# Performance work log

Measured on AMD Instinct MI355X. Metric: run time of the kernel, lower is better.

The kernel has to match this reference:

```python
import jax, jax.numpy as jnp
import numpy as np

H = 4          # num_heads (= num_kv_heads, num_kv_groups = 1)
DK = 256       # head_k_dim
DV = 256       # head_v_dim
M = 256        # num_slots
GATE_NORM = 16.0
EPS = 1e-5


def _rmsnorm(x, w):
    var = jnp.mean(jnp.square(x), axis=-1, keepdims=True)
    return x * jax.lax.rsqrt(var + EPS) * w


def _swish(x):
    return x * jax.nn.sigmoid(x)


def setup_inputs() -> dict:
    key = jax.random.key(0)
    ks = jax.random.split(key, 8)
    B, T, D = 4, 2048, 1024
    scale = 2 ** (-2.5) * (2.0 / (D + D)) ** 0.5 * (3.0 ** 0.5) * 2  # ~xavier*gain magnitude
    return {
        "hidden_states": jax.random.normal(ks[0], (B, T, D), jnp.float32),
        "norm_weight": jnp.ones((D,), jnp.float32),
        "w_q": jax.random.normal(ks[1], (D, D), jnp.float32) * scale,
        "w_k": jax.random.normal(ks[2], (D, D), jnp.float32) * scale,
        "w_v": jax.random.normal(ks[3], (D, D), jnp.float32) * scale,
        "w_f": jax.random.normal(ks[4], (H * M, D), jnp.float32) * scale,
        "gnorm_weight": jnp.ones((D,), jnp.float32),
        "w_o": jax.random.normal(ks[5], (D, D), jnp.float32) * scale,
    }


def _gsa_scan(q, k, v, s, g):
    # all inputs time-major: q [T,B,H,DK], k [T,B,H,DK], v [T,B,H,DV],
    # s [T,B,H,M] (slot write strength), g [T,B,H,M] (log forget gate)
    B, Hh = q.shape[1], q.shape[2]
    Hk0 = jnp.zeros((B, Hh, DK, M), q.dtype)
    Hv0 = jnp.zeros((B, Hh, M, DV), q.dtype)

    def step(carry, xs):
        Hk, Hv = carry
        qt, kt, vt, st, gt = xs
        lam = jnp.exp(gt)                                       # [B,H,M]
        # pass 1: linear attn over slots (gate on value/slot dim)
        Hk = Hk * lam[:, :, None, :] + kt[..., :, None] * st[..., None, :]
        z = jnp.einsum('bhk,bhkm->bhm', qt, Hk)                 # slot logits
        p = jax.nn.softmax(z, axis=-1)                          # slot read weights
        # pass 2: linear attn from slots to values (gate on key/slot dim)
        Hv = Hv * lam[..., :, None] + st[..., :, None] * vt[..., None, :]
        ot = jnp.einsum('bhm,bhmv->bhv', p, Hv)
        return (Hk, Hv), ot

    _, o = jax.lax.scan(step, (Hk0, Hv0), (q, k, v, s, g))
    return o  # [T,B,H,DV]


def reference(hidden_states, norm_weight, w_q, w_k, w_v, w_f, gnorm_weight, w_o):
    B, T, D = hidden_states.shape
    h = _rmsnorm(hidden_states, norm_weight)                    # norm_first
    q = _swish(h @ w_q.T).reshape(B, T, H, DK)                  # swish feature map
    k = _swish(h @ w_k.T).reshape(B, T, H, DK)
    v = _swish(h @ w_v.T).reshape(B, T, H, DV)
    f = jax.nn.log_sigmoid(h @ w_f.T).reshape(B, T, H, M) / GATE_NORM
    s = 1.0 - jnp.exp(f)
    tm = lambda x: jnp.transpose(x, (1, 0, 2, 3))               # [B,T,H,*] -> [T,B,H,*]
    o = _gsa_scan(tm(q), tm(k), tm(v), tm(s), tm(f))            # [T,B,H,DV]
    o = jnp.transpose(o, (1, 0, 2, 3)).reshape(B, T, H * DV)
    # use_norm & no output gate: swish -> RMSNorm -> o_proj
    o = _swish(o)
    o = _rmsnorm(o, gnorm_weight)
    return o @ w_o.T
```

## Files before the change

### kernel.cpp

```cpp
#include <hip/hip_runtime.h>
#include <hip/hip_bf16.h>

typedef unsigned short u16;
typedef unsigned int u32;

using bf16x8 = __bf16 __attribute__((ext_vector_type(8)));
using s16x8  = short  __attribute__((ext_vector_type(8)));
using f32x4  = float  __attribute__((ext_vector_type(4)));

#define DEV static __device__ __forceinline__

constexpr int T_ = 2048, D_ = 1024;
constexpr int C_ = 64, NC_ = 32;
constexpr float EPS_ = 1e-5f;

DEV float bf2f(u16 u) { return __uint_as_float(((u32)u) << 16); }
DEV u16 f2bf(float f) {
  u32 u = __float_as_uint(f);
  return (u16)((u + 0x7fffu + ((u >> 16) & 1u)) >> 16);
}
DEV float swishf(float x) { return x / (1.f + __expf(-x)); }
DEV f32x4 zero4() { f32x4 z = {0.f, 0.f, 0.f, 0.f}; return z; }

DEV bf16x8 ld8(const u16* p, int ld, int r0, int k0, int lane) {
  return *(const bf16x8*)(p + (size_t)(r0 + (lane & 15)) * ld +
                          (size_t)(k0 + ((lane >> 4) << 3)));
}
DEV f32x4 MFMA(bf16x8 a, bf16x8 b, f32x4 c) {
  return __builtin_amdgcn_mfma_f32_16x16x32_bf16(a, b, c, 0, 0, 0);
}
DEV void gld_lds16(const void* g, void* l) {
  __builtin_amdgcn_global_load_lds(
      (const __attribute__((address_space(1))) unsigned int*)g,
      (__attribute__((address_space(3))) unsigned int*)l, 16, 0, 0);
}

__global__ __launch_bounds__(256) void k_cvt5(
    const float* __restrict__ s0, const float* __restrict__ s1,
    const float* __restrict__ s2, const float* __restrict__ s3,
    const float* __restrict__ s4, u16* __restrict__ d0, u16* __restrict__ d1,
    u16* __restrict__ d2, u16* __restrict__ d3, u16* __restrict__ d4) {
  const int wsel = blockIdx.x >> 10;
  const float* s = (wsel == 0) ? s0 : (wsel == 1) ? s1 : (wsel == 2) ? s2
                   : (wsel == 3) ? s3 : s4;
  u16* d = (wsel == 0) ? d0 : (wsel == 1) ? d1 : (wsel == 2) ? d2
           : (wsel == 3) ? d3 : d4;
  const int i = (blockIdx.x & 1023) * 256 + threadIdx.x;
  float4 v = ((const float4*)s)[i];
  uint2 o;
  o.x = (u32)f2bf(v.x) | ((u32)f2bf(v.y) << 16);
  o.y = (u32)f2bf(v.z) | ((u32)f2bf(v.w) << 16);
  ((uint2*)d)[i] = o;
}

__global__ __launch_bounds__(256) void k_rmsnorm(const float* __restrict__ x,
                                                 const float* __restrict__ w,
                                                 u16* __restrict__ h) {
  const int row = blockIdx.x, tid = threadIdx.x;
  float4 v = ((const float4*)(x + (size_t)row * D_))[tid];
  float ss = v.x * v.x + v.y * v.y + v.z * v.z + v.w * v.w;
#pragma unroll
  for (int d = 32; d >= 1; d >>= 1) ss += __shfl_xor(ss, d, 64);
  __shared__ float red[4];
  if ((tid & 63) == 0) red[tid >> 6] = ss;
  __syncthreads();
  float rs = rsqrtf((red[0] + red[1] + red[2] + red[3]) * (1.f / D_) + EPS_);
  float4 wv = ((const float4*)w)[tid];
  uint2 o;
  o.x = (u32)f2bf(v.x * rs * wv.x) | ((u32)f2bf(v.y * rs * wv.y) << 16);
  o.y = (u32)f2bf(v.z * rs * wv.z) | ((u32)f2bf(v.w * rs * wv.w) << 16);
  *(uint2*)(h + (size_t)row * D_ + tid * 4) = o;
}

__global__ __launch_bounds__(256) void k_swishnorm(const u16* __restrict__ x,
                                                   const float* __restrict__ w,
                                                   u16* __restrict__ o) {
  const int row = blockIdx.x, tid = threadIdx.x;
  uint2 pk = *(const uint2*)(x + (size_t)row * D_ + tid * 4);
  float v0 = swishf(bf2f((u16)(pk.x & 0xffff))), v1 = swishf(bf2f((u16)(pk.x >> 16)));
  float v2 = swishf(bf2f((u16)(pk.y & 0xffff))), v3 = swishf(bf2f((u16)(pk.y >> 16)));
  float ss = v0 * v0 + v1 * v1 + v2 * v2 + v3 * v3;
#pragma unroll
  for (int d = 32; d >= 1; d >>= 1) ss += __shfl_xor(ss, d, 64);
  __shared__ float red[4];
  if ((tid & 63) == 0) red[tid >> 6] = ss;
  __syncthreads();
  float rs = rsqrtf((red[0] + red[1] + red[2] + red[3]) * (1.f / D_) + EPS_);
  float4 wv = ((const float4*)w)[tid];
  uint2 ov;
  ov.x = (u32)f2bf(v0 * rs * wv.x) | ((u32)f2bf(v1 * rs * wv.y) << 16);
  ov.y = (u32)f2bf(v2 * rs * wv.z) | ((u32)f2bf(v3 * rs * wv.w) << 16);
  *(uint2*)(o + (size_t)row * D_ + tid * 4) = ov;
}

__global__ __launch_bounds__(256, 2) void k_gemm4(
    const u16* __restrict__ A, const u16* __restrict__ w0,
    const u16* __restrict__ w1, const u16* __restrict__ w2,
    const u16* __restrict__ w3, u16* __restrict__ oq, u16* __restrict__ okk,
    u16* __restrict__ ov, float* __restrict__ og) {
  __shared__ __align__(16) u16 As[128 * 32];
  __shared__ __align__(16) u16 Bs[4][64 * 32];
  const int m0 = blockIdx.x * 128, n0 = blockIdx.y * 64;
  const int tid = threadIdx.x, lane = tid & 63, wvi = tid >> 6;
  f32x4 acc[4][2][4];
#pragma unroll
  for (int w = 0; w < 4; w++)
#pragma unroll
    for (int i = 0; i < 2; i++)
#pragma unroll
      for (int j = 0; j < 4; j++) acc[w][i][j] = zero4();
  const int srow = tid >> 2, scb = (tid & 3) * 8;
  const u16* Ag = A + (size_t)(m0 + srow) * 1024 + scb;
  const u16* Wg0 = w0 + (size_t)(n0 + srow) * 1024 + scb;
  const u16* Wg1 = w1 + (size_t)(n0 + srow) * 1024 + scb;
  const u16* Wg2 = w2 + (size_t)(n0 + srow) * 1024 + scb;
  const u16* Wg3 = w3 + (size_t)(n0 + srow) * 1024 + scb;
  u16* AsW = As + (wvi * 16) * 32;
  const int bofs = (wvi * 16) * 32;
  for (int kk = 0; kk < 1024; kk += 32) {
    gld_lds16(Ag + kk, AsW);
    gld_lds16(Ag + kk + 64 * 1024, AsW + 64 * 32);
    gld_lds16(Wg0 + kk, Bs[0] + bofs);
    gld_lds16(Wg1 + kk, Bs[1] + bofs);
    gld_lds16(Wg2 + kk, Bs[2] + bofs);
    gld_lds16(Wg3 + kk, Bs[3] + bofs);
    __syncthreads();
    bf16x8 af[2];
#pragma unroll
    for (int i = 0; i < 2; i++) af[i] = ld8(As, 32, wvi * 32 + 16 * i, 0, lane);
#pragma unroll
    for (int w = 0; w < 4; w++) {
      bf16x8 bfr[4];
#pragma unroll
      for (int j = 0; j < 4; j++) bfr[j] = ld8(Bs[w], 32, 16 * j, 0, lane);
#pragma unroll
      for (int i = 0; i < 2; i++)
#pragma unroll
        for (int j = 0; j < 4; j++) acc[w][i][j] = MFMA(af[i], bfr[j], acc[w][i][j]);
    }
    __syncthreads();
  }
  const int q4 = lane >> 4, c15 = lane & 15;
#pragma unroll
  for (int w = 0; w < 4; w++)
#pragma unroll
    for (int i = 0; i < 2; i++)
#pragma unroll
      for (int j = 0; j < 4; j++)
#pragma unroll
        for (int r = 0; r < 4; r++) {
          int grow = m0 + wvi * 32 + 16 * i + 4 * q4 + r;
          int gcol = n0 + 16 * j + c15;
          size_t idx = (size_t)grow * 1024 + gcol;
          float val = acc[w][i][j][r];
          if (w < 3) {
            u16* o = (w == 0) ? oq : (w == 1) ? okk : ov;
            o[idx] = f2bf(swishf(val));
          } else {
            float g = (val >= 0.f) ? -log1pf(__expf(-val))
                                   : (val - log1pf(__expf(val)));
            og[idx] = g * (1.0f / 16.0f);
          }
        }
}

__global__ __launch_bounds__(256) void k_gemmO(const u16* __restrict__ A,
                                               const u16* __restrict__ W,
                                               float* __restrict__ ofin) {
  __shared__ __align__(16) u16 As[128 * 32];
  __shared__ __align__(16) u16 Bs[128 * 32];
  const int m0 = blockIdx.x * 128, n0 = blockIdx.y * 128;
  const int tid = threadIdx.x, lane = tid & 63, wvi = tid >> 6;
  const int wr = wvi >> 1, wc = wvi & 1;
  f32x4 acc[4][4];
#pragma unroll
  for (int i = 0; i < 4; i++)
#pragma unroll
    for (int j = 0; j < 4; j++) acc[i][j] = zero4();
  const int srow = tid >> 2, scb = (tid & 3) * 8;
  const u16* Ag = A + (size_t)(m0 + srow) * 1024 + scb;
  const u16* Wg = W + (size_t)(n0 + srow) * 1024 + scb;
  u16* AsW = As + (wvi * 16) * 32;
  u16* BsW = Bs + (wvi * 16) * 32;
  for (int kk = 0; kk < 1024; kk += 32) {
    gld_lds16(Ag + kk, AsW);
    gld_lds16(Ag + kk + 64 * 1024, AsW + 64 * 32);
    gld_lds16(Wg + kk, BsW);
    gld_lds16(Wg + kk + 64 * 1024, BsW + 64 * 32);
    __syncthreads();
    bf16x8 af[4], bfr[4];
#pragma unroll
    for (int i = 0; i < 4; i++) af[i] = ld8(As, 32, wr * 64 + 16 * i, 0, lane);
#pragma unroll
    for (int j = 0; j < 4; j++) bfr[j] = ld8(Bs, 32, wc * 64 + 16 * j, 0, lane);
#pragma unroll
    for (int i = 0; i < 4; i++)
#pragma unroll
      for (int j = 0; j < 4; j++) acc[i][j] = MFMA(af[i], bfr[j], acc[i][j]);
    __syncthreads();
  }
  const int q4 = lane >> 4, c15 = lane & 15;
#pragma unroll
  for (int i = 0; i < 4; i++)
#pragma unroll
    for (int j = 0; j < 4; j++)
#pragma unroll
      for (int r = 0; r < 4; r++) {
        int grow = m0 + wr * 64 + 16 * i + 4 * q4 + r;
        int gcol = n0 + wc * 64 + 16 * j + c15;
        ofin[(size_t)grow * 1024 + gcol] = acc[i][j][r];
      }
}

__global__ __launch_bounds__(256) void k_gates(float* __restrict__ g_inout,
                                               u16* __restrict__ U_t,
                                               float* __restrict__ Lam) {
  const int c = blockIdx.x, p = blockIdx.y, tid = threadIdx.x;
  const int b = p >> 2, hh = p & 3;
  const int R0 = b * T_ + c * C_, hb = hh * 256;
  float ga = 0.f, ea = 1.f;
  short ubuf[C_];
#pragma unroll
  for (int t = 0; t < C_; t++) {
    size_t gi = (size_t)(R0 + t) * D_ + hb + tid;
    float gv = g_inout[gi];
    ga += gv;
    ea = __expf(ga);
    ubuf[t] = (short)f2bf((1.f - __expf(gv)) * __expf(-ga));
    g_inout[gi] = ea;
  }
  Lam[((size_t)p * NC_ + c) * 256 + tid] = ea;
  u16* up = U_t + ((size_t)p * NC_ + c) * (256 * C_) + (size_t)tid * C_;
#pragma unroll
  for (int i = 0; i < 8; i++) {
    s16x8 w;
#pragma unroll
    for (int j = 0; j < 8; j++) w[j] = ubuf[i * 8 + j];
    *(s16x8*)(up + i * 8) = w;
  }
}

__global__ __launch_bounds__(256) void k_intra(
    const u16* __restrict__ kg, const u16* __restrict__ vg,
    const u16* __restrict__ U_t, const float* __restrict__ Lam,
    u16* __restrict__ Sk, u16* __restrict__ Sv) {
  __shared__ __align__(16) u16 KV[256 * 72];
  __shared__ float LamH[256];
  const int c = blockIdx.x, p = blockIdx.y;
  const int b = p >> 2, hh = p & 3;
  const int R0 = b * T_ + c * C_, hb = hh * 256;
  const int tid = threadIdx.x, lane = tid & 63, wvi = tid >> 6;
  const int q4 = lane >> 4, c15 = lane & 15;
  const size_t chunk = (size_t)p * NC_ + c;
  const u16* Uc = U_t + chunk * (256 * C_);
  const size_t scBase = chunk * (256 * 256);

  LamH[tid] = Lam[chunk * 256 + tid];
  for (int t = 0; t < C_; t++)
    KV[tid * 72 + t] = kg[(size_t)(R0 + t) * D_ + hb + tid];
  __syncthreads();

  for (int cb = 0; cb < 4; cb++) {
    f32x4 acc[4][4];
#pragma unroll
    for (int i = 0; i < 4; i++)
#pragma unroll
      for (int j = 0; j < 4; j++) acc[i][j] = zero4();
#pragma unroll
    for (int ks = 0; ks < 2; ks++) {
      bf16x8 af[4], bfr[4];
#pragma unroll
      for (int i = 0; i < 4; i++) af[i] = ld8(Uc, C_, 64 * wvi + 16 * i, 32 * ks, lane);
#pragma unroll
      for (int j = 0; j < 4; j++) bfr[j] = ld8(KV, 72, 64 * cb + 16 * j, 32 * ks, lane);
#pragma unroll
      for (int i = 0; i < 4; i++)
#pragma unroll
        for (int j = 0; j < 4; j++) acc[i][j] = MFMA(af[i], bfr[j], acc[i][j]);
    }
#pragma unroll
    for (int i = 0; i < 4; i++)
#pragma unroll
      for (int j = 0; j < 4; j++)
#pragma unroll
        for (int r = 0; r < 4; r++) {
          int ml = 64 * wvi + 16 * i + 4 * q4 + r;
          int dd = 64 * cb + 16 * j + c15;
          Sk[scBase + (size_t)ml * 256 + dd] = f2bf(acc[i][j][r] * LamH[ml]);
        }
  }
  __syncthreads();

  for (int t = 0; t < C_; t++)
    KV[tid * 72 + t] = vg[(size_t)(R0 + t) * D_ + hb + tid];
  __syncthreads();

  for (int cb = 0; cb < 4; cb++) {
    f32x4 acc[4][4];
#pragma unroll
    for (int i = 0; i < 4; i++)
#pragma unroll
      for (int j = 0; j < 4; j++) acc[i][j] = zero4();
#pragma unroll
    for (int ks = 0; ks < 2; ks++) {
      bf16x8 af[4], bfr[4];
#pragma unroll
      for (int i = 0; i < 4; i++) af[i] = ld8(KV, 72, 64 * wvi + 16 * i, 32 * ks, lane);
#pragma unroll
      for (int j = 0; j < 4; j++) bfr[j] = ld8(Uc, C_, 64 * cb + 16 * j, 32 * ks, lane);
#pragma unroll
      for (int i = 0; i < 4; i++)
#pragma unroll
        for (int j = 0; j < 4; j++) acc[i][j] = MFMA(af[i], bfr[j], acc[i][j]);
    }
#pragma unroll
    for (int i = 0; i < 4; i++)
#pragma unroll
      for (int j = 0; j < 4; j++)
#pragma unroll
        for (int r = 0; r < 4; r++) {
          int vv = 64 * wvi + 16 * i + 4 * q4 + r;
          int ml = 64 * cb + 16 * j + c15;
          Sv[scBase + (size_t)vv * 256 + ml] = f2bf(acc[i][j][r] * LamH[ml]);
        }
  }
}

__global__ __launch_bounds__(256) void k_scan(u16* __restrict__ Sk,
                                              u16* __restrict__ Sv,
                                              const float* __restrict__ Lam) {
  const int gid = blockIdx.x * 256 + threadIdx.x;
  const int st = gid >> 17;
  const int w = gid & 131071;
  const int p = w >> 13;
  const int r = (w >> 5) & 255;
  const int c0 = (w & 31) * 8;
  u16* S = st ? Sv : Sk;
  const size_t base = (size_t)p * NC_ * 65536 + (size_t)r * 256 + c0;
  const float* Lp = Lam + (size_t)p * NC_ * 256;
  float acc[8] = {0, 0, 0, 0, 0, 0, 0, 0};
  for (int c = 0; c < NC_; c++) {
    s16x8 in = *(const s16x8*)(S + base + (size_t)c * 65536);
    s16x8 ov;
#pragma unroll
    for (int j = 0; j < 8; j++) ov[j] = (short)f2bf(acc[j]);
    *(s16x8*)(S + base + (size_t)c * 65536) = ov;
    if (st == 0) {
      float lam = Lp[c * 256 + r];
#pragma unroll
      for (int j = 0; j < 8; j++) acc[j] = acc[j] * lam + bf2f((u16)in[j]);
    } else {
#pragma unroll
      for (int j = 0; j < 8; j++) {
        float lam = Lp[c * 256 + c0 + j];
        acc[j] = acc[j] * lam + bf2f((u16)in[j]);
      }
    }
  }
}

__global__ __launch_bounds__(256) void k_out(
    const u16* __restrict__ qg, const u16* __restrict__ kg,
    const u16* __restrict__ vg, const u16* __restrict__ U_t,
    const float* __restrict__ Eg, const u16* __restrict__ Sk,
    const u16* __restrict__ Sv, u16* __restrict__ orw) {
  __shared__ __align__(16) char lds[61440];
  u16* As = (u16*)lds;
  u16* Pt = (u16*)(lds + 9216);
  u16* UnH = (u16*)(lds + 43008);
  u16* VxH = (u16*)(lds + 43008);

  const int c = blockIdx.x, p = blockIdx.y;
  const int b = p >> 2, hh = p & 3;
  const int R0 = b * T_ + c * C_, hb = hh * 256;
  const int tid = threadIdx.x, lane = tid & 63, wvi = tid >> 6;
  const int q4 = lane >> 4, c15 = lane & 15;
  const u16* qbase = qg + (size_t)R0 * D_ + hb;
  const u16* kbase = kg + (size_t)R0 * D_ + hb;
  const float* Ebase = Eg + (size_t)R0 * D_ + hb;
  const size_t chunk = (size_t)p * NC_ + c;
  const u16* SkC = Sk + chunk * 65536;
  const u16* SvC = Sv + chunk * 65536;
  const u16* Uc = U_t + chunk * (256 * C_);

  {
    f32x4 acc[4];
#pragma unroll
    for (int n = 0; n < 4; n++) acc[n] = zero4();
#pragma unroll
    for (int ks = 0; ks < 8; ks++) {
      bf16x8 af = ld8(qbase, D_, 16 * wvi, 32 * ks, lane);
#pragma unroll
      for (int n = 0; n < 4; n++)
        acc[n] = MFMA(af, ld8(kbase, D_, 16 * n, 32 * ks, lane), acc[n]);
    }
#pragma unroll
    for (int n = 0; n < 4; n++)
#pragma unroll
      for (int r = 0; r < 4; r++) {
        int t = 16 * wvi + 4 * q4 + r, tau = 16 * n + c15;
        As[t * 72 + tau] = f2bf(tau <= t ? acc[n][r] : 0.f);
      }
  }
  __syncthreads();

  f32x4 zac[16], eRg[16];
#pragma unroll
  for (int mh = 0; mh < 2; mh++) {
#pragma unroll
    for (int n = 0; n < 8; n++) zac[mh * 8 + n] = zero4();
#pragma unroll
    for (int ks = 0; ks < 2; ks++) {
      bf16x8 af = ld8(As, 72, 16 * wvi, 32 * ks, lane);
#pragma unroll
      for (int n = 0; n < 8; n++)
        zac[mh * 8 + n] = MFMA(af, ld8(Uc, C_, mh * 128 + 16 * n, 32 * ks, lane),
                               zac[mh * 8 + n]);
    }
#pragma unroll
    for (int ks = 0; ks < 8; ks++) {
      bf16x8 af = ld8(qbase, D_, 16 * wvi, 32 * ks, lane);
#pragma unroll
      for (int n = 0; n < 8; n++)
        zac[mh * 8 + n] = MFMA(
            af, ld8(SkC + (size_t)mh * 128 * 256, 256, 16 * n, 32 * ks, lane),
            zac[mh * 8 + n]);
    }
#pragma unroll
    for (int n = 0; n < 8; n++)
#pragma unroll
      for (int r = 0; r < 4; r++) {
        int t = 16 * wvi + 4 * q4 + r;
        float e = Ebase[(size_t)t * D_ + mh * 128 + 16 * n + c15];
        eRg[mh * 8 + n][r] = e;
        zac[mh * 8 + n][r] *= e;
      }
  }

#pragma unroll
  for (int r = 0; r < 4; r++) {
    float mx = -3.0e38f;
#pragma unroll
    for (int i = 0; i < 16; i++) mx = fmaxf(mx, zac[i][r]);
    mx = fmaxf(mx, __shfl_xor(mx, 1, 64));
    mx = fmaxf(mx, __shfl_xor(mx, 2, 64));
    mx = fmaxf(mx, __shfl_xor(mx, 4, 64));
    mx = fmaxf(mx, __shfl_xor(mx, 8, 64));
    float sm = 0.f;
#pragma unroll
    for (int i = 0; i < 16; i++) {
      float e = __expf(zac[i][r] - mx);
      zac[i][r] = e;
      sm += e;
    }
    sm += __shfl_xor(sm, 1, 64);
    sm += __shfl_xor(sm, 2, 64);
    sm += __shfl_xor(sm, 4, 64);
    sm += __shfl_xor(sm, 8, 64);
    float inv = 1.f / sm;
#pragma unroll
    for (int i = 0; i < 16; i++) zac[i][r] *= inv * eRg[i][r];
  }
#pragma unroll
  for (int i = 0; i < 16; i++)
#pragma unroll
    for (int r = 0; r < 4; r++) {
      int t = 16 * wvi + 4 * q4 + r;
      int m = (i >> 3) * 128 + 16 * (i & 7) + c15;
      Pt[t * 264 + m] = f2bf(zac[i][r]);
    }
  __syncthreads();

  {
    f32x4 wac[4];
#pragma unroll
    for (int n = 0; n < 4; n++) wac[n] = zero4();
    for (int mh = 0; mh < 2; mh++) {
      {
        int mloc = tid >> 1, th = tid & 1;
        const u16* ur = Uc + (size_t)(mh * 128 + mloc) * C_ + th * 32;
#pragma unroll
        for (int tt = 0; tt < 4; tt++) {
          s16x8 v = *(const s16x8*)(ur + tt * 8);
#pragma unroll
          for (int j = 0; j < 8; j++)
            UnH[(th * 32 + tt * 8 + j) * 132 + mloc] = (u16)v[j];
        }
      }
      __syncthreads();
#pragma unroll
      for (int ks = 0; ks < 4; ks++) {
        bf16x8 af = ld8(Pt, 264, 16 * wvi, mh * 128 + 32 * ks, lane);
#pragma unroll
        for (int n = 0; n < 4; n++)
          wac[n] = MFMA(af, ld8(UnH, 132, 16 * n, 32 * ks, lane), wac[n]);
      }
      __syncthreads();
    }
#pragma unroll
    for (int n = 0; n < 4; n++)
#pragma unroll
      for (int r = 0; r < 4; r++) {
        int t = 16 * wvi + 4 * q4 + r, tau = 16 * n + c15;
        As[t * 72 + tau] = f2bf(tau <= t ? wac[n][r] : 0.f);
      }
  }
  __syncthreads();

  for (int vh = 0; vh < 2; vh++) {
    {
      int vloc = tid >> 1, th = tid & 1;
#pragma unroll 4
      for (int tt = 0; tt < 32; tt++) {
        int t = th * 32 + tt;
        VxH[vloc * 72 + t] = vg[(size_t)(R0 + t) * D_ + hb + vh * 128 + vloc];
      }
    }
    __syncthreads();
    f32x4 oac[8];
#pragma unroll
    for (int n = 0; n < 8; n++) oac[n] = zero4();
#pragma unroll
    for (int ks = 0; ks < 8; ks++) {
      bf16x8 af = ld8(Pt, 264, 16 * wvi, 32 * ks, lane);
#pragma unroll
      for (int n = 0; n < 8; n++)
        oac[n] = MFMA(af, ld8(SvC + (size_t)vh * 128 * 256, 256, 16 * n, 32 * ks, lane), oac[n]);
    }
#pragma unroll
    for (int ks = 0; ks < 2; ks++) {
      bf16x8 af = ld8(As, 72, 16 * wvi, 32 * ks, lane);
#pragma unroll
      for (int n = 0; n < 8; n++)
        oac[n] = MFMA(af, ld8(VxH, 72, 16 * n, 32 * ks, lane), oac[n]);
    }
#pragma unroll
    for (int n = 0; n < 8; n++)
#pragma unroll
      for (int r = 0; r < 4; r++) {
        int t = 16 * wvi + 4 * q4 + r;
        int vc = vh * 128 + 16 * n + c15;
        orw[(size_t)(R0 + t) * D_ + hb + vc] = f2bf(oac[n][r]);
      }
    __syncthreads();
  }
}

extern "C" void kernel_launch(void* const* d_in, const int* in_sizes, int n_in,
                              void* d_out, int out_size, void* d_ws, size_t ws_size,
                              hipStream_t stream) {
  (void)in_sizes; (void)n_in; (void)out_size; (void)ws_size;
  const float* x   = (const float*)d_in[0];
  const float* nw  = (const float*)d_in[1];
  const float* wq  = (const float*)d_in[2];
  const float* wk  = (const float*)d_in[3];
  const float* wvp = (const float*)d_in[4];
  const float* wf  = (const float*)d_in[5];
  const float* gw  = (const float*)d_in[6];
  const float* wo  = (const float*)d_in[7];
  float* out = (float*)d_out;
  char* ws = (char*)d_ws;
  const size_t MB = 1024ull * 1024ull;
  u16*   hbuf = (u16*)(ws);
  u16*   qb   = (u16*)(ws + 16 * MB);
  u16*   kb   = (u16*)(ws + 32 * MB);
  u16*   vb   = (u16*)(ws + 48 * MB);
  float* gb   = (float*)(ws + 64 * MB);
  u16*   SkB  = (u16*)(ws + 96 * MB);
  u16*   SvB  = (u16*)(ws + 160 * MB);
  float* Lam  = (float*)(ws + 224 * MB);
  u16*   orw  = (u16*)(ws + 226 * MB);
  u16*   wqb  = (u16*)(ws + 242 * MB);
  u16*   wkb  = (u16*)(ws + 244 * MB);
  u16*   wvb  = (u16*)(ws + 246 * MB);
  u16*   wfb  = (u16*)(ws + 248 * MB);
  u16*   wob  = (u16*)(ws + 250 * MB);
  u16*   U_t  = hbuf;

  k_cvt5<<<dim3(5120), dim3(256), 0, stream>>>(wq, wk, wvp, wf, wo,
                                               wqb, wkb, wvb, wfb, wob);
  k_rmsnorm<<<dim3(8192), dim3(256), 0, stream>>>(x, nw, hbuf);
  k_gemm4<<<dim3(64, 16), dim3(256), 0, stream>>>(
      hbuf, wqb, wkb, wvb, wfb, qb, kb, vb, gb);
  k_gates<<<dim3(NC_, 16), dim3(256), 0, stream>>>(gb, U_t, Lam);
  k_intra<<<dim3(NC_, 16), dim3(256), 0, stream>>>(kb, vb, U_t, Lam, SkB, SvB);
  k_scan<<<dim3(1024), dim3(256), 0, stream>>>(SkB, SvB, Lam);
  k_out<<<dim3(NC_, 16), dim3(256), 0, stream>>>(qb, kb, vb, U_t, gb, SkB, SvB, orw);
  k_swishnorm<<<dim3(8192), dim3(256), 0, stream>>>(orw, gw, hbuf);
  k_gemmO<<<dim3(64, 8), dim3(256), 0, stream>>>(hbuf, wob, out);
}
```

Baseline: 481.0 us.

## Split fused QKVF GEMM into per-weight 128x128 tiles with 2x2 wave layout

```diff
diff --git a/kernel.cpp b/kernel.cpp
--- a/kernel.cpp
+++ b/kernel.cpp
@@ -93,75 +93,66 @@
   *(uint2*)(o + (size_t)row * D_ + tid * 4) = ov;
 }
 
-__global__ __launch_bounds__(256, 2) void k_gemm4(
+__global__ __launch_bounds__(256) void k_gemm4f(
     const u16* __restrict__ A, const u16* __restrict__ w0,
     const u16* __restrict__ w1, const u16* __restrict__ w2,
     const u16* __restrict__ w3, u16* __restrict__ oq, u16* __restrict__ okk,
     u16* __restrict__ ov, float* __restrict__ og) {
   __shared__ __align__(16) u16 As[128 * 32];
-  __shared__ __align__(16) u16 Bs[4][64 * 32];
-  const int m0 = blockIdx.x * 128, n0 = blockIdx.y * 64;
+  __shared__ __align__(16) u16 Bs[128 * 32];
+  const int m0 = blockIdx.x * 128;
+  const int wsel = blockIdx.y >> 3;
+  const int n0 = (blockIdx.y & 7) * 128;
+  const u16* W = (wsel == 0) ? w0 : (wsel == 1) ? w1 : (wsel == 2) ? w2 : w3;
   const int tid = threadIdx.x, lane = tid & 63, wvi = tid >> 6;
-  f32x4 acc[4][2][4];
-#pragma unroll
-  for (int w = 0; w < 4; w++)
-#pragma unroll
-    for (int i = 0; i < 2; i++)
-#pragma unroll
-      for (int j = 0; j < 4; j++) acc[w][i][j] = zero4();
+  const int wr = wvi >> 1, wc = wvi & 1;
+  f32x4 acc[4][4];
+#pragma unroll
+  for (int i = 0; i < 4; i++)
+#pragma unroll
+    for (int j = 0; j < 4; j++) acc[i][j] = zero4();
   const int srow = tid >> 2, scb = (tid & 3) * 8;
   const u16* Ag = A + (size_t)(m0 + srow) * 1024 + scb;
-  const u16* Wg0 = w0 + (size_t)(n0 + srow) * 1024 + scb;
-  const u16* Wg1 = w1 + (size_t)(n0 + srow) * 1024 + scb;
-  const u16* Wg2 = w2 + (size_t)(n0 + srow) * 1024 + scb;
-  const u16* Wg3 = w3 + (size_t)(n0 + srow) * 1024 + scb;
+  const u16* Wg = W + (size_t)(n0 + srow) * 1024 + scb;
   u16* AsW = As + (wvi * 16) * 32;
-  const int bofs = (wvi * 16) * 32;
+  u16* BsW = Bs + (wvi * 16) * 32;
   for (int kk = 0; kk < 1024; kk += 32) {
     gld_lds16(Ag + kk, AsW);
     gld_lds16(Ag + kk + 64 * 1024, AsW + 64 * 32);
-    gld_lds16(Wg0 + kk, Bs[0] + bofs);
-    gld_lds16(Wg1 + kk, Bs[1] + bofs);
-    gld_lds16(Wg2 + kk, Bs[2] + bofs);
-    gld_lds16(Wg3 + kk, Bs[3] + bofs);
+    gld_lds16(Wg + kk, BsW);
+    gld_lds16(Wg + kk + 64 * 1024, BsW + 64 * 32);
     __syncthreads();
-    bf16x8 af[2];
-#pragma unroll
-    for (int i = 0; i < 2; i++) af[i] = ld8(As, 32, wvi * 32 + 16 * i, 0, lane);
-#pragma unroll
-    for (int w = 0; w < 4; w++) {
-      bf16x8 bfr[4];
-#pragma unroll
-      for (int j = 0; j < 4; j++) bfr[j] = ld8(Bs[w], 32, 16 * j, 0, lane);
-#pragma unroll
-      for (int i = 0; i < 2; i++)
-#pragma unroll
-        for (int j = 0; j < 4; j++) acc[w][i][j] = MFMA(af[i], bfr[j], acc[w][i][j]);
-    }
+    bf16x8 af[4], bfr[4];
+#pragma unroll
+    for (int i = 0; i < 4; i++) af[i] = ld8(As, 32, wr * 64 + 16 * i, 0, lane);
+#pragma unroll
+    for (int j = 0; j < 4; j++) bfr[j] = ld8(Bs, 32, wc * 64 + 16 * j, 0, lane);
+#pragma unroll
+    for (int i = 0; i < 4; i++)
+#pragma unroll
+      for (int j = 0; j < 4; j++) acc[i][j] = MFMA(af[i], bfr[j], acc[i][j]);
     __syncthreads();
   }
   const int q4 = lane >> 4, c15 = lane & 15;
-#pragma unroll
-  for (int w = 0; w < 4; w++)
-#pragma unroll
-    for (int i = 0; i < 2; i++)
-#pragma unroll
-      for (int j = 0; j < 4; j++)
-#pragma unroll
-        for (int r = 0; r < 4; r++) {
-          int grow = m0 + wvi * 32 + 16 * i + 4 * q4 + r;
-          int gcol = n0 + 16 * j + c15;
-          size_t idx = (size_t)grow * 1024 + gcol;
-          float val = acc[w][i][j][r];
-          if (w < 3) {
-            u16* o = (w == 0) ? oq : (w == 1) ? okk : ov;
-            o[idx] = f2bf(swishf(val));
-          } else {
-            float g = (val >= 0.f) ? -log1pf(__expf(-val))
-                                   : (val - log1pf(__expf(val)));
-            og[idx] = g * (1.0f / 16.0f);
-          }
+  u16* obf = (wsel == 0) ? oq : (wsel == 1) ? okk : ov;
+#pragma unroll
+  for (int i = 0; i < 4; i++)
+#pragma unroll
+    for (int j = 0; j < 4; j++)
+#pragma unroll
+      for (int r = 0; r < 4; r++) {
+        int grow = m0 + wr * 64 + 16 * i + 4 * q4 + r;
+        int gcol = n0 + wc * 64 + 16 * j + c15;
+        size_t idx = (size_t)grow * 1024 + gcol;
+        float val = acc[i][j][r];
+        if (wsel < 3) {
+          obf[idx] = f2bf(swishf(val));
+        } else {
+          float g = (val >= 0.f) ? -log1pf(__expf(-val))
+                                 : (val - log1pf(__expf(val)));
+          og[idx] = g * (1.0f / 16.0f);
         }
+      }
 }
 
 __global__ __launch_bounds__(256) void k_gemmO(const u16* __restrict__ A,
@@ -580,7 +571,7 @@
   k_cvt5<<<dim3(5120), dim3(256), 0, stream>>>(wq, wk, wvp, wf, wo,
                                                wqb, wkb, wvb, wfb, wob);
   k_rmsnorm<<<dim3(8192), dim3(256), 0, stream>>>(x, nw, hbuf);
-  k_gemm4<<<dim3(64, 16), dim3(256), 0, stream>>>(
+  k_gemm4f<<<dim3(64, 32), dim3(256), 0, stream>>>(
       hbuf, wqb, wkb, wvb, wfb, qb, kb, vb, gb);
   k_gates<<<dim3(NC_, 16), dim3(256), 0, stream>>>(gb, U_t, Lam);
   k_intra<<<dim3(NC_, 16), dim3(256), 0, stream>>>(kb, vb, U_t, Lam, SkB, SvB);
```

Result: slower. 531.9 us (+10.6%).
